# Performance work log

Measured on AMD Instinct MI355X. Metric: run time of the kernel, lower is better.

The kernel has to match this reference:

```python
import jax, jax.numpy as jnp
import numpy as np

LN_EPS = 1e-12


def setup_inputs() -> dict:
    key = jax.random.key(0)
    ks = jax.random.split(key, 5)
    B, N, D_IN, D_OUT, E = 32, 2048, 128, 128, 64
    return {
        "x": jax.random.normal(ks[0], (B, N, D_IN), dtype=jnp.float32),
        "node_embeddings": jax.random.normal(ks[1], (N, E), dtype=jnp.float32),
        "time_embeddings": jax.random.normal(ks[2], (E,), dtype=jnp.float32),
        "weights_pool": jax.random.normal(ks[3], (E, 2, D_IN, D_OUT), dtype=jnp.float32) * 0.02,
        "bias_pool": jax.random.normal(ks[4], (E, D_OUT), dtype=jnp.float32) * 0.02,
        "ln_weight": jnp.ones((E,), dtype=jnp.float32),
        "ln_bias": jnp.zeros((E,), dtype=jnp.float32),
    }


def reference(x, node_embeddings, time_embeddings, weights_pool, bias_pool, ln_weight, ln_bias):
    # e: [N, E] = LayerNorm(node_emb + time_emb)  (dropout in eval mode = identity)
    e = node_embeddings + time_embeddings[None, :]
    mu = jnp.mean(e, axis=-1, keepdims=True)
    var = jnp.mean(jnp.square(e - mu), axis=-1, keepdims=True)
    e = (e - mu) * jax.lax.rsqrt(var + LN_EPS) * ln_weight + ln_bias

    # adaptive adjacency: softmax over rows of e @ e.T  -> [N, N]
    adj = jax.nn.softmax(jnp.einsum('nd,md->nm', e, e), axis=1)

    # per-node weights [N, 2, I, O] and bias [N, O]
    weights = jnp.einsum('nd,dkio->nkio', e, weights_pool)
    bias = e @ bias_pool  # [N, O]

    # supports: k=0 identity (x itself), k=1 adjacency aggregation
    x_agg = jnp.einsum('nm,bmc->bnc', adj, x)        # [B, N, I]
    x_g = jnp.stack([x, x_agg], axis=2)              # [B, N, 2, I]

    # per-node batched GEMM + bias
    out = jnp.einsum('bnki,nkio->bno', x_g, weights) + bias
    return out
```

## Files before the change

### kernel.cpp

```cpp
#include <hip/hip_runtime.h>


typedef unsigned short u16;
typedef unsigned int u32;
typedef __attribute__((ext_vector_type(8))) short bf16x8;
typedef __attribute__((ext_vector_type(4))) float f32x4;
typedef const __attribute__((address_space(1))) u16* gas1;
typedef __attribute__((address_space(3))) u16* las3;

#define NN 2048
#define EE 64
#define CC 128
#define BB 32

__device__ __forceinline__ u16 f2bf(float f) {
  u32 u = __builtin_bit_cast(u32, f);
  u += 0x7fffu + ((u >> 16) & 1u);
  return (u16)(u >> 16);
}

__device__ __forceinline__ f32x4 mfma16(bf16x8 a, bf16x8 b, f32x4 c) {
  return __builtin_amdgcn_mfma_f32_16x16x32_bf16(a, b, c, 0, 0, 0);
}

__global__ __launch_bounds__(64) void k_prep(
    const float* __restrict__ ne, const float* __restrict__ te,
    const float* __restrict__ lnw, const float* __restrict__ lnb,
    const float* __restrict__ bias_pool,
    float* __restrict__ e, u16* __restrict__ e_bf, float* __restrict__ bias_out) {
  int n = blockIdx.x;
  int d = threadIdx.x;
  float v = ne[n * EE + d] + te[d];
  float s = v;
#pragma unroll
  for (int off = 32; off > 0; off >>= 1) s += __shfl_xor(s, off);
  float mean = s * (1.0f / 64.0f);
  float c = v - mean;
  float q = c * c;
#pragma unroll
  for (int off = 32; off > 0; off >>= 1) q += __shfl_xor(q, off);
  float inv = rsqrtf(q * (1.0f / 64.0f) + 1e-12f);
  float ev = c * inv * lnw[d] + lnb[d];
  e[n * EE + d] = ev;
  e_bf[n * EE + d] = f2bf(ev);
  __shared__ float sh[64];
  sh[d] = ev;
  __syncthreads();
#pragma unroll
  for (int oo = 0; oo < 2; ++oo) {
    int o = oo * 64 + d;
    float acc = 0.f;
#pragma unroll 8
    for (int dd = 0; dd < 64; ++dd) acc += sh[dd] * bias_pool[dd * CC + o];
    bias_out[n * CC + o] = acc;
  }
}

__global__ __launch_bounds__(256) void k_poolt(const float* __restrict__ pool,
                                               u16* __restrict__ pool_r) {
  __shared__ float t[128 * 65];
  int ki = blockIdx.x;
  int tid = threadIdx.x;
  for (int it = 0; it < 32; ++it) {
    int idx = it * 256 + tid;
    int d = idx >> 7, o = idx & 127;
    t[o * 65 + d] = pool[d * 32768 + ki * 128 + o];
  }
  __syncthreads();
  for (int it = 0; it < 32; ++it) {
    int idx = it * 256 + tid;
    int o = idx >> 6, d = idx & 63;
    pool_r[((size_t)o * 256 + ki) * 64 + d] = f2bf(t[o * 65 + d]);
  }
}

__global__ __launch_bounds__(256) void k_xtrans(const float* __restrict__ x,
                                                u16* __restrict__ x_t,
                                                u16* __restrict__ xg_t) {
  __shared__ u16 t[128 * 68];
  int b = blockIdx.x >> 5;
  int m0 = (blockIdx.x & 31) * 64;
  int tid = threadIdx.x;
  for (int it = 0; it < 32; ++it) {
    int idx = it * 256 + tid;
    int m = idx >> 7, c = idx & 127;
    float v = x[((size_t)b * NN + m0 + m) * CC + c];
    t[c * 68 + m] = f2bf(v);
  }
  __syncthreads();
  for (int it = 0; it < 32; ++it) {
    int idx = it * 256 + tid;
    int c = idx >> 6, m = idx & 63;
    x_t[((size_t)b * CC + c) * NN + m0 + m] = t[c * 68 + m];
  }
  for (int it = 0; it < 16; ++it) {
    int idx = it * 256 + tid;
    int m = idx >> 6, c2 = idx & 63;
    float2 v = *(const float2*)&x[((size_t)b * NN + m0 + m) * CC + c2 * 2];
    u32 pk = (u32)f2bf(v.x) | ((u32)f2bf(v.y) << 16);
    *(u32*)&xg_t[(((size_t)(m0 + m)) * 32 + b) * 256 + c2 * 2] = pk;
  }
}

__global__ __launch_bounds__(256) void k_Sexp(const float* __restrict__ e,
                                              u16* __restrict__ P,
                                              float* __restrict__ rs) {
  extern __shared__ float sm[];
  float* er = sm;
  float* ec = sm + 128 * 68;
  int n0 = (blockIdx.x >> 4) * 128, m0 = (blockIdx.x & 15) * 128;
  int tid = threadIdx.x;
  for (int it = 0; it < 32; ++it) {
    int idx = it * 256 + tid;
    int r = idx >> 6, d = idx & 63;
    er[r * 68 + d] = e[(n0 + r) * EE + d];
    ec[r * 68 + d] = e[(m0 + r) * EE + d];
  }
  __syncthreads();
  int tx = tid & 15, ty = tid >> 4;
  float acc[8][8] = {};
  for (int d4 = 0; d4 < 64; d4 += 4) {
    f32x4 av[8], bv[8];
#pragma unroll
    for (int i = 0; i < 8; ++i) av[i] = *(const f32x4*)&er[(ty + 16 * i) * 68 + d4];
#pragma unroll
    for (int j = 0; j < 8; ++j) bv[j] = *(const f32x4*)&ec[(tx + 16 * j) * 68 + d4];
#pragma unroll
    for (int i = 0; i < 8; ++i)
#pragma unroll
      for (int j = 0; j < 8; ++j) {
        acc[i][j] += av[i][0] * bv[j][0];
        acc[i][j] += av[i][1] * bv[j][1];
        acc[i][j] += av[i][2] * bv[j][2];
        acc[i][j] += av[i][3] * bv[j][3];
      }
  }
#pragma unroll
  for (int i = 0; i < 8; ++i) {
    float s = 0.f;
#pragma unroll
    for (int j = 0; j < 8; ++j) {
      float pv = __expf(acc[i][j]);
      P[(size_t)(n0 + ty + 16 * i) * NN + m0 + tx + 16 * j] = f2bf(pv);
      s += pv;
    }
#pragma unroll
    for (int off = 8; off > 0; off >>= 1) s += __shfl_xor(s, off);
    if (tx == 0) atomicAdd(&rs[n0 + ty + 16 * i], s);
  }
}

__global__ __launch_bounds__(256, 3) void k_aggr(const u16* __restrict__ P,
                                                 const u16* __restrict__ x_t,
                                                 const float* __restrict__ rs,
                                                 u16* __restrict__ xg_t) {
  __shared__ u16 As[128 * 64];
  __shared__ u16 Bs[128 * 64];
  int mb = blockIdx.x & 15, b = blockIdx.x >> 4;
  int n0 = mb * 128;
  int tid = threadIdx.x;
  int lane = tid & 63, w = tid >> 6;
  int wm = w >> 1, wn = w & 1;
  int lm = lane & 15, lq = lane >> 4;
  f32x4 acc[4][4] = {};
  const u16* a_src = P + (size_t)n0 * NN;
  const u16* b_src = x_t + (size_t)b * CC * NN;
  for (int kc = 0; kc < NN; kc += 64) {
    __syncthreads();
#pragma unroll
    for (int ii = 0; ii < 4; ++ii) {
      int idx = ii * 256 + tid;
      int row = idx >> 3, ch = idx & 7;
      __builtin_amdgcn_global_load_lds((gas1)(a_src + (size_t)row * NN + kc + ch * 8),
                                       (las3)(As + (size_t)(ii * 256 + w * 64) * 8), 16, 0, 0);
      __builtin_amdgcn_global_load_lds((gas1)(b_src + (size_t)row * NN + kc + ch * 8),
                                       (las3)(Bs + (size_t)(ii * 256 + w * 64) * 8), 16, 0, 0);
    }
    __syncthreads();
#pragma unroll
    for (int kk = 0; kk < 64; kk += 32) {
      bf16x8 af[4], bq[4];
#pragma unroll
      for (int i = 0; i < 4; ++i)
        af[i] = *(const bf16x8*)&As[(wm * 64 + i * 16 + lm) * 64 + kk + lq * 8];
#pragma unroll
      for (int j = 0; j < 4; ++j)
        bq[j] = *(const bf16x8*)&Bs[(wn * 64 + j * 16 + lm) * 64 + kk + lq * 8];
#pragma unroll
      for (int i = 0; i < 4; ++i)
#pragma unroll
        for (int j = 0; j < 4; ++j)
          acc[i][j] = mfma16(af[i], bq[j], acc[i][j]);
    }
  }
#pragma unroll
  for (int i = 0; i < 4; ++i) {
    int nr = n0 + wm * 64 + i * 16 + lq * 4;
#pragma unroll
    for (int r = 0; r < 4; ++r) {
      float sc = 1.0f / rs[nr + r];
#pragma unroll
      for (int j = 0; j < 4; ++j) {
        int c = wn * 64 + j * 16 + lm;
        xg_t[((size_t)(nr + r) * 32 + b) * 256 + 128 + c] = f2bf(acc[i][j][r] * sc);
      }
    }
  }
}

__global__ __launch_bounds__(256, 2) void k_gen(const u16* __restrict__ e_bf,
                                                const u16* __restrict__ pool_r,
                                                u16* __restrict__ W_t) {
  __shared__ u16 Tl[64 * 264];
  int cb = blockIdx.x & 127, nb = blockIdx.x >> 7;
  int c0 = cb * 256, n0 = nb * 64;
  int tid = threadIdx.x;
  int lane = tid & 63, w = tid >> 6;
  int lm = lane & 15, lq = lane >> 4;
  bf16x8 eB[4][2];
#pragma unroll
  for (int nt = 0; nt < 4; ++nt)
#pragma unroll
    for (int ks = 0; ks < 2; ++ks)
      eB[nt][ks] = *(const bf16x8*)&e_bf[(n0 + nt * 16 + lm) * EE + ks * 32 + lq * 8];
#pragma unroll
  for (int ct = 0; ct < 4; ++ct) {
    int ctile = w * 4 + ct;
    const u16* ap = pool_r + ((size_t)c0 + ctile * 16 + lm) * 64 + lq * 8;
    bf16x8 pA0 = *(const bf16x8*)ap;
    bf16x8 pA1 = *(const bf16x8*)(ap + 32);
#pragma unroll
    for (int nt = 0; nt < 4; ++nt) {
      f32x4 g = {0.f, 0.f, 0.f, 0.f};
      g = mfma16(pA0, eB[nt][0], g);
      g = mfma16(pA1, eB[nt][1], g);
      ushort4 h;
      h.x = f2bf(g[0]); h.y = f2bf(g[1]); h.z = f2bf(g[2]); h.w = f2bf(g[3]);
      *(ushort4*)&Tl[(nt * 16 + lm) * 264 + ctile * 16 + lq * 4] = h;
    }
  }
  __syncthreads();
#pragma unroll
  for (int it = 0; it < 8; ++it) {
    int idx = it * 256 + tid;
    int node = idx >> 5, seg = idx & 31;
    uint4 v = *(const uint4*)&Tl[node * 264 + seg * 8];
    *(uint4*)&W_t[(size_t)(n0 + node) * 32768 + c0 + seg * 8] = v;
  }
}

__global__ __launch_bounds__(256, 3) void k_apply(const u16* __restrict__ xg_t,
                                                  const u16* __restrict__ W_t,
                                                  const float* __restrict__ bias,
                                                  float* __restrict__ out) {
  int n0 = blockIdx.x * 2;
  int tid = threadIdx.x;
  int lane = tid & 63, w = tid >> 6;
  int lm = lane & 15, lq = lane >> 4;
  int n = n0 + (w & 1), oh = w >> 1;
  const u16* xb = xg_t + (size_t)n * 32 * 256;
  const u16* wb = W_t + (size_t)n * 32768 + (size_t)oh * 64 * 256;
  f32x4 acc[2][4] = {};
#pragma unroll
  for (int ks = 0; ks < 8; ++ks) {
    int ko = ks * 32 + lq * 8;
    bf16x8 a0 = *(const bf16x8*)&xb[lm * 256 + ko];
    bf16x8 a1 = *(const bf16x8*)&xb[(16 + lm) * 256 + ko];
#pragma unroll
    for (int ot = 0; ot < 4; ++ot) {
      bf16x8 bv = *(const bf16x8*)&wb[(ot * 16 + lm) * 256 + ko];
      acc[0][ot] = mfma16(a0, bv, acc[0][ot]);
      acc[1][ot] = mfma16(a1, bv, acc[1][ot]);
    }
  }
#pragma unroll
  for (int ot = 0; ot < 4; ++ot) {
    int oc = oh * 64 + ot * 16 + lm;
    float bv = bias[n * CC + oc];
#pragma unroll
    for (int mt = 0; mt < 2; ++mt)
#pragma unroll
      for (int r = 0; r < 4; ++r) {
        int b = mt * 16 + lq * 4 + r;
        out[((size_t)b * NN + n) * CC + oc] = acc[mt][ot][r] + bv;
      }
  }
}

extern "C" void kernel_launch(void* const* d_in, const int* in_sizes, int n_in,
                              void* d_out, int out_size, void* d_ws, size_t ws_size,
                              hipStream_t stream) {
  const float* x        = (const float*)d_in[0];
  const float* node_emb = (const float*)d_in[1];
  const float* time_emb = (const float*)d_in[2];
  const float* pool     = (const float*)d_in[3];
  const float* bias_pl  = (const float*)d_in[4];
  const float* ln_w     = (const float*)d_in[5];
  const float* ln_b     = (const float*)d_in[6];
  float* out = (float*)d_out;

  char* p = (char*)d_ws;
  auto alloc = [&](size_t bytes) {
    char* r = p;
    p += (bytes + 255) & ~(size_t)255;
    return r;
  };
  float* e      = (float*)alloc((size_t)NN * EE * 4);
  u16*   e_bf   = (u16*)  alloc((size_t)NN * EE * 2);
  float* biasb  = (float*)alloc((size_t)NN * CC * 4);
  u16*   Pm     = (u16*)  alloc((size_t)NN * NN * 2);
  float* rs     = (float*)alloc((size_t)NN * 4);
  u16*   x_t    = (u16*)  alloc((size_t)BB * CC * NN * 2);
  u16*   xg_t   = (u16*)  alloc((size_t)NN * BB * 256 * 2);
  u16*   pool_r = (u16*)  alloc((size_t)128 * 256 * 64 * 2);
  u16*   W_t    = (u16*)  alloc((size_t)NN * 32768 * 2);

  if (ws_size < (size_t)(p - (char*)d_ws)) return;

  (void)hipFuncSetAttribute((const void*)k_Sexp, hipFuncAttributeMaxDynamicSharedMemorySize,
                            2 * 128 * 68 * 4);
  (void)hipMemsetAsync(rs, 0, (size_t)NN * 4, stream);

  k_prep<<<NN, 64, 0, stream>>>(node_emb, time_emb, ln_w, ln_b, bias_pl, e, e_bf, biasb);
  k_poolt<<<256, 256, 0, stream>>>(pool, pool_r);
  k_xtrans<<<BB * 32, 256, 0, stream>>>(x, x_t, xg_t);
  k_gen<<<128 * 32, 256, 0, stream>>>(e_bf, pool_r, W_t);
  k_Sexp<<<256, 256, 2 * 128 * 68 * 4, stream>>>(e, Pm, rs);
  k_aggr<<<16 * BB, 256, 0, stream>>>(Pm, x_t, rs, xg_t);
  k_apply<<<NN / 2, 256, 0, stream>>>(xg_t, W_t, biasb, out);
}
```

Baseline: 265.5 us.

## Merge independent prep and GEMM kernels into horizontally fused launches

Combines the LayerNorm/bias, pool transpose, and x transpose kernels into one launch that dispatches on block index. It also fuses the adjacency aggregation GEMM with the per-node weight generation into one launch so the two can share the GPU. The Sexp tile shrinks from 128x128 to 64x64 to give 1024 blocks instead of 256. This removes launch gaps and tail underutilization, at the cost of mixed register and LDS pressure within the fused kernels and the occupancy hint changing to 4.

```diff
diff --git a/kernel.cpp b/kernel.cpp
--- a/kernel.cpp
+++ b/kernel.cpp
@@ -23,94 +23,92 @@
   return __builtin_amdgcn_mfma_f32_16x16x32_bf16(a, b, c, 0, 0, 0);
 }
 
-__global__ __launch_bounds__(64) void k_prep(
-    const float* __restrict__ ne, const float* __restrict__ te,
-    const float* __restrict__ lnw, const float* __restrict__ lnb,
-    const float* __restrict__ bias_pool,
-    float* __restrict__ e, u16* __restrict__ e_bf, float* __restrict__ bias_out) {
-  int n = blockIdx.x;
-  int d = threadIdx.x;
-  float v = ne[n * EE + d] + te[d];
-  float s = v;
-#pragma unroll
-  for (int off = 32; off > 0; off >>= 1) s += __shfl_xor(s, off);
-  float mean = s * (1.0f / 64.0f);
-  float c = v - mean;
-  float q = c * c;
-#pragma unroll
-  for (int off = 32; off > 0; off >>= 1) q += __shfl_xor(q, off);
-  float inv = rsqrtf(q * (1.0f / 64.0f) + 1e-12f);
-  float ev = c * inv * lnw[d] + lnb[d];
-  e[n * EE + d] = ev;
-  e_bf[n * EE + d] = f2bf(ev);
-  __shared__ float sh[64];
-  sh[d] = ev;
-  __syncthreads();
-#pragma unroll
-  for (int oo = 0; oo < 2; ++oo) {
-    int o = oo * 64 + d;
-    float acc = 0.f;
+__global__ __launch_bounds__(256) void k_mega0(
+    const float* __restrict__ x, const float* __restrict__ ne,
+    const float* __restrict__ te, const float* __restrict__ pool,
+    const float* __restrict__ bias_pool, const float* __restrict__ lnw,
+    const float* __restrict__ lnb,
+    float* __restrict__ e, u16* __restrict__ e_bf, float* __restrict__ bias_out,
+    u16* __restrict__ pool_r, u16* __restrict__ x_t, u16* __restrict__ xg_t) {
+  __shared__ __align__(16) char smem[33280];
+  int bid = blockIdx.x;
+  int tid = threadIdx.x;
+  if (bid < 512) {
+    float* sh = (float*)smem;
+    int nw = tid >> 6, d = tid & 63;
+    int n = bid * 4 + nw;
+    float v = ne[n * EE + d] + te[d];
+    float s = v;
+#pragma unroll
+    for (int off = 32; off > 0; off >>= 1) s += __shfl_xor(s, off);
+    float mean = s * (1.0f / 64.0f);
+    float c = v - mean;
+    float q = c * c;
+#pragma unroll
+    for (int off = 32; off > 0; off >>= 1) q += __shfl_xor(q, off);
+    float inv = rsqrtf(q * (1.0f / 64.0f) + 1e-12f);
+    float ev = c * inv * lnw[d] + lnb[d];
+    e[n * EE + d] = ev;
+    e_bf[n * EE + d] = f2bf(ev);
+    sh[nw * 64 + d] = ev;
+    __syncthreads();
+#pragma unroll
+    for (int oo = 0; oo < 2; ++oo) {
+      int o = oo * 64 + d;
+      float acc = 0.f;
 #pragma unroll 8
-    for (int dd = 0; dd < 64; ++dd) acc += sh[dd] * bias_pool[dd * CC + o];
-    bias_out[n * CC + o] = acc;
-  }
-}
-
-__global__ __launch_bounds__(256) void k_poolt(const float* __restrict__ pool,
-                                               u16* __restrict__ pool_r) {
-  __shared__ float t[128 * 65];
-  int ki = blockIdx.x;
-  int tid = threadIdx.x;
-  for (int it = 0; it < 32; ++it) {
-    int idx = it * 256 + tid;
-    int d = idx >> 7, o = idx & 127;
-    t[o * 65 + d] = pool[d * 32768 + ki * 128 + o];
-  }
-  __syncthreads();
-  for (int it = 0; it < 32; ++it) {
-    int idx = it * 256 + tid;
-    int o = idx >> 6, d = idx & 63;
-    pool_r[((size_t)o * 256 + ki) * 64 + d] = f2bf(t[o * 65 + d]);
-  }
-}
-
-__global__ __launch_bounds__(256) void k_xtrans(const float* __restrict__ x,
-                                                u16* __restrict__ x_t,
-                                                u16* __restrict__ xg_t) {
-  __shared__ u16 t[128 * 68];
-  int b = blockIdx.x >> 5;
-  int m0 = (blockIdx.x & 31) * 64;
-  int tid = threadIdx.x;
-  for (int it = 0; it < 32; ++it) {
-    int idx = it * 256 + tid;
-    int m = idx >> 7, c = idx & 127;
-    float v = x[((size_t)b * NN + m0 + m) * CC + c];
-    t[c * 68 + m] = f2bf(v);
-  }
-  __syncthreads();
-  for (int it = 0; it < 32; ++it) {
-    int idx = it * 256 + tid;
-    int c = idx >> 6, m = idx & 63;
-    x_t[((size_t)b * CC + c) * NN + m0 + m] = t[c * 68 + m];
-  }
-  for (int it = 0; it < 16; ++it) {
-    int idx = it * 256 + tid;
-    int m = idx >> 6, c2 = idx & 63;
-    float2 v = *(const float2*)&x[((size_t)b * NN + m0 + m) * CC + c2 * 2];
-    u32 pk = (u32)f2bf(v.x) | ((u32)f2bf(v.y) << 16);
-    *(u32*)&xg_t[(((size_t)(m0 + m)) * 32 + b) * 256 + c2 * 2] = pk;
+      for (int dd = 0; dd < 64; ++dd) acc += sh[nw * 64 + dd] * bias_pool[dd * CC + o];
+      bias_out[n * CC + o] = acc;
+    }
+  } else if (bid < 768) {
+    float* t = (float*)smem;
+    int ki = bid - 512;
+    for (int it = 0; it < 32; ++it) {
+      int idx = it * 256 + tid;
+      int d = idx >> 7, o = idx & 127;
+      t[o * 65 + d] = pool[d * 32768 + ki * 128 + o];
+    }
+    __syncthreads();
+    for (int it = 0; it < 32; ++it) {
+      int idx = it * 256 + tid;
+      int o = idx >> 6, d = idx & 63;
+      pool_r[((size_t)o * 256 + ki) * 64 + d] = f2bf(t[o * 65 + d]);
+    }
+  } else {
+    u16* t = (u16*)smem;
+    int bx = bid - 768;
+    int b = bx >> 5;
+    int m0 = (bx & 31) * 64;
+    for (int it = 0; it < 32; ++it) {
+      int idx = it * 256 + tid;
+      int m = idx >> 7, c = idx & 127;
+      float v = x[((size_t)b * NN + m0 + m) * CC + c];
+      t[c * 68 + m] = f2bf(v);
+    }
+    __syncthreads();
+    for (int it = 0; it < 32; ++it) {
+      int idx = it * 256 + tid;
+      int c = idx >> 6, m = idx & 63;
+      x_t[((size_t)b * CC + c) * NN + m0 + m] = t[c * 68 + m];
+    }
+    for (int it = 0; it < 16; ++it) {
+      int idx = it * 256 + tid;
+      int m = idx >> 6, c2 = idx & 63;
+      float2 v = *(const float2*)&x[((size_t)b * NN + m0 + m) * CC + c2 * 2];
+      u32 pk = (u32)f2bf(v.x) | ((u32)f2bf(v.y) << 16);
+      *(u32*)&xg_t[(((size_t)(m0 + m)) * 32 + b) * 256 + c2 * 2] = pk;
+    }
   }
 }
 
 __global__ __launch_bounds__(256) void k_Sexp(const float* __restrict__ e,
                                               u16* __restrict__ P,
                                               float* __restrict__ rs) {
-  extern __shared__ float sm[];
-  float* er = sm;
-  float* ec = sm + 128 * 68;
-  int n0 = (blockIdx.x >> 4) * 128, m0 = (blockIdx.x & 15) * 128;
+  __shared__ float er[64 * 68];
+  __shared__ float ec[64 * 68];
+  int n0 = (blockIdx.x >> 5) * 64, m0 = (blockIdx.x & 31) * 64;
   int tid = threadIdx.x;
-  for (int it = 0; it < 32; ++it) {
+  for (int it = 0; it < 16; ++it) {
     int idx = it * 256 + tid;
     int r = idx >> 6, d = idx & 63;
     er[r * 68 + d] = e[(n0 + r) * EE + d];
@@ -118,17 +116,17 @@
   }
   __syncthreads();
   int tx = tid & 15, ty = tid >> 4;
-  float acc[8][8] = {};
+  float acc[4][4] = {};
   for (int d4 = 0; d4 < 64; d4 += 4) {
-    f32x4 av[8], bv[8];
-#pragma unroll
-    for (int i = 0; i < 8; ++i) av[i] = *(const f32x4*)&er[(ty + 16 * i) * 68 + d4];
-#pragma unroll
-    for (int j = 0; j < 8; ++j) bv[j] = *(const f32x4*)&ec[(tx + 16 * j) * 68 + d4];
-#pragma unroll
-    for (int i = 0; i < 8; ++i)
-#pragma unroll
-      for (int j = 0; j < 8; ++j) {
+    f32x4 av[4], bv[4];
+#pragma unroll
+    for (int i = 0; i < 4; ++i) av[i] = *(const f32x4*)&er[(ty + 16 * i) * 68 + d4];
+#pragma unroll
+    for (int j = 0; j < 4; ++j) bv[j] = *(const f32x4*)&ec[(tx + 16 * j) * 68 + d4];
+#pragma unroll
+    for (int i = 0; i < 4; ++i)
+#pragma unroll
+      for (int j = 0; j < 4; ++j) {
         acc[i][j] += av[i][0] * bv[j][0];
         acc[i][j] += av[i][1] * bv[j][1];
         acc[i][j] += av[i][2] * bv[j][2];
@@ -136,10 +134,10 @@
       }
   }
 #pragma unroll
-  for (int i = 0; i < 8; ++i) {
+  for (int i = 0; i < 4; ++i) {
     float s = 0.f;
 #pragma unroll
-    for (int j = 0; j < 8; ++j) {
+    for (int j = 0; j < 4; ++j) {
       float pv = __expf(acc[i][j]);
       P[(size_t)(n0 + ty + 16 * i) * NN + m0 + tx + 16 * j] = f2bf(pv);
       s += pv;
@@ -150,102 +148,100 @@
   }
 }
 
-__global__ __launch_bounds__(256, 3) void k_aggr(const u16* __restrict__ P,
-                                                 const u16* __restrict__ x_t,
-                                                 const float* __restrict__ rs,
-                                                 u16* __restrict__ xg_t) {
-  __shared__ u16 As[128 * 64];
-  __shared__ u16 Bs[128 * 64];
-  int mb = blockIdx.x & 15, b = blockIdx.x >> 4;
-  int n0 = mb * 128;
-  int tid = threadIdx.x;
-  int lane = tid & 63, w = tid >> 6;
-  int wm = w >> 1, wn = w & 1;
-  int lm = lane & 15, lq = lane >> 4;
-  f32x4 acc[4][4] = {};
-  const u16* a_src = P + (size_t)n0 * NN;
-  const u16* b_src = x_t + (size_t)b * CC * NN;
-  for (int kc = 0; kc < NN; kc += 64) {
-    __syncthreads();
-#pragma unroll
-    for (int ii = 0; ii < 4; ++ii) {
-      int idx = ii * 256 + tid;
-      int row = idx >> 3, ch = idx & 7;
-      __builtin_amdgcn_global_load_lds((gas1)(a_src + (size_t)row * NN + kc + ch * 8),
-                                       (las3)(As + (size_t)(ii * 256 + w * 64) * 8), 16, 0, 0);
-      __builtin_amdgcn_global_load_lds((gas1)(b_src + (size_t)row * NN + kc + ch * 8),
-                                       (las3)(Bs + (size_t)(ii * 256 + w * 64) * 8), 16, 0, 0);
-    }
-    __syncthreads();
-#pragma unroll
-    for (int kk = 0; kk < 64; kk += 32) {
-      bf16x8 af[4], bq[4];
-#pragma unroll
-      for (int i = 0; i < 4; ++i)
-        af[i] = *(const bf16x8*)&As[(wm * 64 + i * 16 + lm) * 64 + kk + lq * 8];
-#pragma unroll
-      for (int j = 0; j < 4; ++j)
-        bq[j] = *(const bf16x8*)&Bs[(wn * 64 + j * 16 + lm) * 64 + kk + lq * 8];
-#pragma unroll
-      for (int i = 0; i < 4; ++i)
-#pragma unroll
-        for (int j = 0; j < 4; ++j)
-          acc[i][j] = mfma16(af[i], bq[j], acc[i][j]);
-    }
-  }
-#pragma unroll
-  for (int i = 0; i < 4; ++i) {
-    int nr = n0 + wm * 64 + i * 16 + lq * 4;
-#pragma unroll
-    for (int r = 0; r < 4; ++r) {
-      float sc = 1.0f / rs[nr + r];
-#pragma unroll
-      for (int j = 0; j < 4; ++j) {
-        int c = wn * 64 + j * 16 + lm;
-        xg_t[((size_t)(nr + r) * 32 + b) * 256 + 128 + c] = f2bf(acc[i][j][r] * sc);
-      }
-    }
-  }
-}
-
-__global__ __launch_bounds__(256, 2) void k_gen(const u16* __restrict__ e_bf,
-                                                const u16* __restrict__ pool_r,
-                                                u16* __restrict__ W_t) {
-  __shared__ u16 Tl[64 * 264];
-  int cb = blockIdx.x & 127, nb = blockIdx.x >> 7;
-  int c0 = cb * 256, n0 = nb * 64;
+__global__ __launch_bounds__(256, 4) void k_mega2(
+    const u16* __restrict__ P, const u16* __restrict__ x_t,
+    const float* __restrict__ rs, u16* __restrict__ xg_t,
+    const u16* __restrict__ e_bf, const u16* __restrict__ pool_r,
+    u16* __restrict__ W_t) {
+  __shared__ __align__(16) char smem[33792];
   int tid = threadIdx.x;
   int lane = tid & 63, w = tid >> 6;
   int lm = lane & 15, lq = lane >> 4;
-  bf16x8 eB[4][2];
-#pragma unroll
-  for (int nt = 0; nt < 4; ++nt)
-#pragma unroll
-    for (int ks = 0; ks < 2; ++ks)
-      eB[nt][ks] = *(const bf16x8*)&e_bf[(n0 + nt * 16 + lm) * EE + ks * 32 + lq * 8];
-#pragma unroll
-  for (int ct = 0; ct < 4; ++ct) {
-    int ctile = w * 4 + ct;
-    const u16* ap = pool_r + ((size_t)c0 + ctile * 16 + lm) * 64 + lq * 8;
-    bf16x8 pA0 = *(const bf16x8*)ap;
-    bf16x8 pA1 = *(const bf16x8*)(ap + 32);
-#pragma unroll
-    for (int nt = 0; nt < 4; ++nt) {
-      f32x4 g = {0.f, 0.f, 0.f, 0.f};
-      g = mfma16(pA0, eB[nt][0], g);
-      g = mfma16(pA1, eB[nt][1], g);
-      ushort4 h;
-      h.x = f2bf(g[0]); h.y = f2bf(g[1]); h.z = f2bf(g[2]); h.w = f2bf(g[3]);
-      *(ushort4*)&Tl[(nt * 16 + lm) * 264 + ctile * 16 + lq * 4] = h;
-    }
-  }
-  __syncthreads();
-#pragma unroll
-  for (int it = 0; it < 8; ++it) {
-    int idx = it * 256 + tid;
-    int node = idx >> 5, seg = idx & 31;
-    uint4 v = *(const uint4*)&Tl[node * 264 + seg * 8];
-    *(uint4*)&W_t[(size_t)(n0 + node) * 32768 + c0 + seg * 8] = v;
+  if (blockIdx.x < 512) {
+    u16* As = (u16*)smem;
+    u16* Bs = (u16*)(smem + 16384);
+    int mb = blockIdx.x & 15, b = blockIdx.x >> 4;
+    int n0 = mb * 128;
+    int wm = w >> 1, wn = w & 1;
+    f32x4 acc[4][4] = {};
+    const u16* a_src = P + (size_t)n0 * NN;
+    const u16* b_src = x_t + (size_t)b * CC * NN;
+    for (int kc = 0; kc < NN; kc += 64) {
+      __syncthreads();
+#pragma unroll
+      for (int ii = 0; ii < 4; ++ii) {
+        int idx = ii * 256 + tid;
+        int row = idx >> 3, ch = idx & 7;
+        __builtin_amdgcn_global_load_lds((gas1)(a_src + (size_t)row * NN + kc + ch * 8),
+                                         (las3)(As + (size_t)(ii * 256 + w * 64) * 8), 16, 0, 0);
+        __builtin_amdgcn_global_load_lds((gas1)(b_src + (size_t)row * NN + kc + ch * 8),
+                                         (las3)(Bs + (size_t)(ii * 256 + w * 64) * 8), 16, 0, 0);
+      }
+      __syncthreads();
+#pragma unroll
+      for (int kk = 0; kk < 64; kk += 32) {
+        bf16x8 af[4], bq[4];
+#pragma unroll
+        for (int i = 0; i < 4; ++i)
+          af[i] = *(const bf16x8*)&As[(wm * 64 + i * 16 + lm) * 64 + kk + lq * 8];
+#pragma unroll
+        for (int j = 0; j < 4; ++j)
+          bq[j] = *(const bf16x8*)&Bs[(wn * 64 + j * 16 + lm) * 64 + kk + lq * 8];
+#pragma unroll
+        for (int i = 0; i < 4; ++i)
+#pragma unroll
+          for (int j = 0; j < 4; ++j)
+            acc[i][j] = mfma16(af[i], bq[j], acc[i][j]);
+      }
+    }
+#pragma unroll
+    for (int i = 0; i < 4; ++i) {
+      int nr = n0 + wm * 64 + i * 16 + lq * 4;
+#pragma unroll
+      for (int r = 0; r < 4; ++r) {
+        float sc = 1.0f / rs[nr + r];
+#pragma unroll
+        for (int j = 0; j < 4; ++j) {
+          int c = wn * 64 + j * 16 + lm;
+          xg_t[((size_t)(nr + r) * 32 + b) * 256 + 128 + c] = f2bf(acc[i][j][r] * sc);
+        }
+      }
+    }
+  } else {
+    u16* Tl = (u16*)smem;
+    int bid = blockIdx.x - 512;
+    int cb = bid & 127, nb = bid >> 7;
+    int c0 = cb * 256, n0 = nb * 64;
+    bf16x8 eB[4][2];
+#pragma unroll
+    for (int nt = 0; nt < 4; ++nt)
+#pragma unroll
+      for (int ks = 0; ks < 2; ++ks)
+        eB[nt][ks] = *(const bf16x8*)&e_bf[(n0 + nt * 16 + lm) * EE + ks * 32 + lq * 8];
+#pragma unroll
+    for (int ct = 0; ct < 4; ++ct) {
+      int ctile = w * 4 + ct;
+      const u16* ap = pool_r + ((size_t)c0 + ctile * 16 + lm) * 64 + lq * 8;
+      bf16x8 pA0 = *(const bf16x8*)ap;
+      bf16x8 pA1 = *(const bf16x8*)(ap + 32);
+#pragma unroll
+      for (int nt = 0; nt < 4; ++nt) {
+        f32x4 g = {0.f, 0.f, 0.f, 0.f};
+        g = mfma16(pA0, eB[nt][0], g);
+        g = mfma16(pA1, eB[nt][1], g);
+        ushort4 h;
+        h.x = f2bf(g[0]); h.y = f2bf(g[1]); h.z = f2bf(g[2]); h.w = f2bf(g[3]);
+        *(ushort4*)&Tl[(nt * 16 + lm) * 264 + ctile * 16 + lq * 4] = h;
+      }
+    }
+    __syncthreads();
+#pragma unroll
+    for (int it = 0; it < 8; ++it) {
+      int idx = it * 256 + tid;
+      int node = idx >> 5, seg = idx & 31;
+      uint4 v = *(const uint4*)&Tl[node * 264 + seg * 8];
+      *(uint4*)&W_t[(size_t)(n0 + node) * 32768 + c0 + seg * 8] = v;
+    }
   }
 }
 
@@ -317,15 +313,11 @@
 
   if (ws_size < (size_t)(p - (char*)d_ws)) return;
 
-  (void)hipFuncSetAttribute((const void*)k_Sexp, hipFuncAttributeMaxDynamicSharedMemorySize,
-                            2 * 128 * 68 * 4);
   (void)hipMemsetAsync(rs, 0, (size_t)NN * 4, stream);
 
-  k_prep<<<NN, 64, 0, stream>>>(node_emb, time_emb, ln_w, ln_b, bias_pl, e, e_bf, biasb);
-  k_poolt<<<256, 256, 0, stream>>>(pool, pool_r);
-  k_xtrans<<<BB * 32, 256, 0, stream>>>(x, x_t, xg_t);
-  k_gen<<<128 * 32, 256, 0, stream>>>(e_bf, pool_r, W_t);
-  k_Sexp<<<256, 256, 2 * 128 * 68 * 4, stream>>>(e, Pm, rs);
-  k_aggr<<<16 * BB, 256, 0, stream>>>(Pm, x_t, rs, xg_t);
+  k_mega0<<<1792, 256, 0, stream>>>(x, node_emb, time_emb, pool, bias_pl, ln_w, ln_b,
+                                    e, e_bf, biasb, pool_r, x_t, xg_t);
+  k_Sexp<<<1024, 256, 0, stream>>>(e, Pm, rs);
+  k_mega2<<<4608, 256, 0, stream>>>(Pm, x_t, rs, xg_t, e_bf, pool_r, W_t);
   k_apply<<<NN / 2, 256, 0, stream>>>(xg_t, W_t, biasb, out);
 }
```

Result: faster. 238.0 us (-10.3%).
